# Kernel optimization log

Hardware: AMD Instinct MI355X
Metric: run time of the kernel (lower is better)

The kernel has to match this reference:

```python
import jax, jax.numpy as jnp
import numpy as np

B, N, C, ORDER, COORD, K = 2, 4096, 64, 4, 2, 8
EPS = 1e-8
LN_EPS = 1e-6


def _layer_norm(x, scale, bias):
    mu = jnp.mean(x, axis=-1, keepdims=True)
    var = jnp.mean(jnp.square(x - mu), axis=-1, keepdims=True)
    return (x - mu) * jax.lax.rsqrt(var + LN_EPS) * scale + bias


def _multipole(x, positions, W, order_scales, ln_s, ln_b):
    # stability clamping / NaN masking as in the original
    x = jnp.where(jnp.isnan(x), 0.0, jnp.clip(x, -1e6, 1e6))
    p = jnp.where(jnp.isnan(positions), 0.0, jnp.clip(positions, -1e6, 1e6))
    r = jnp.maximum(jnp.linalg.norm(p, axis=-1, keepdims=True), EPS)  # (B,N,1)
    theta = jnp.arctan2(p[..., 1], p[..., 0] + EPS)  # (B,N)
    per_order = []
    for o in range(ORDER + 1):
        r_o = r ** o
        radial = jnp.tanh(r_o / (1.0 + r_o))          # (B,N,1)
        angular = jnp.cos(o * theta)                    # (B,N)
        mc = x * radial * angular[..., None]            # (B,N,C)
        nm = mc / (jnp.linalg.norm(mc, axis=-1, keepdims=True) + EPS)
        scale = jnp.clip(order_scales[o], 0.01, 1.0)
        per_order.append(nm * scale / (o + 1.0))
    M = jnp.stack(per_order, axis=-1)  # (B,N,C,O+1) per-order weighted moments
    # per-order linear maps, summed over orders (evident intent of (C,C,O+1) weights)
    transformed = jnp.einsum('bnio,ijo->bnj', M, W)
    normalized = _layer_norm(transformed, ln_s, ln_b)
    return jnp.where(jnp.isnan(normalized), x, normalized)


def _local_messages(x, positions, W1, b1, W2, b2):
    # full pairwise distances, then kNN (exclude self)
    d = jnp.linalg.norm(positions[:, :, None, :] - positions[:, None, :, :], axis=-1)  # (B,N,N)
    _, idx = jax.lax.top_k(-d, K + 1)
    nbr = idx[:, :, 1:]  # (B,N,K)
    # gather neighbor features without materializing (B,N,N,C)
    nbr_feat = jax.vmap(lambda xb, ib: xb[ib])(x, nbr)           # (B,N,K,C)
    self_feat = jnp.broadcast_to(x[:, :, None, :], nbr_feat.shape)
    comb = jnp.concatenate([self_feat, nbr_feat], axis=-1)       # (B,N,K,2C)
    msg = jax.nn.gelu(comb @ W1 + b1) @ W2 + b2                  # (B,N,K,C)
    return jnp.mean(msg, axis=2)


def reference(x, positions, multipole_weights, order_scales, mp_ln_scale, mp_ln_bias,
              msg_W1, msg_b1, msg_W2, msg_b2, upd_W1, upd_b1, upd_W2, upd_b2,
              out_ln_scale, out_ln_bias):
    mp = _multipole(x, positions, multipole_weights, order_scales, mp_ln_scale, mp_ln_bias)
    lm = _local_messages(x, positions, msg_W1, msg_b1, msg_W2, msg_b2)
    u = jnp.concatenate([mp, lm], axis=-1)                       # (B,N,2C)
    upd = jax.nn.gelu(u @ upd_W1 + upd_b1) @ upd_W2 + upd_b2     # (B,N,C)
    return _layer_norm(x + upd, out_ln_scale, out_ln_bias)


def setup_inputs() -> dict:
    key = jax.random.key(0)
    ks = jax.random.split(key, 8)
    C2 = 2 * C
    xav = lambda k, shp: jax.random.normal(k, shp) * np.float32(np.sqrt(2.0 / (shp[0] + shp[-1])))
    return {
        'x': jax.random.normal(ks[0], (B, N, C), dtype=jnp.float32),
        'positions': jax.random.normal(ks[1], (B, N, COORD), dtype=jnp.float32),
        'multipole_weights': jax.random.normal(ks[2], (C, C, ORDER + 1)) * np.float32(0.1 / np.sqrt(ORDER + 1) * np.sqrt(1.0 / C)),
        'order_scales': jnp.ones(ORDER + 1) * 0.1,
        'mp_ln_scale': jnp.ones(C), 'mp_ln_bias': jnp.zeros(C),
        'msg_W1': xav(ks[3], (C2, C)), 'msg_b1': jnp.zeros(C),
        'msg_W2': xav(ks[4], (C, C)), 'msg_b2': jnp.zeros(C),
        'upd_W1': xav(ks[5], (C2, C2)), 'upd_b1': jnp.zeros(C2),
        'upd_W2': xav(ks[6], (C2, C)), 'upd_b2': jnp.zeros(C),
        'out_ln_scale': jnp.ones(C), 'out_ln_bias': jnp.zeros(C),
    }
```

## Files before the change

kernel.cpp:

```cpp
#include <hip/hip_runtime.h>
#include <math.h>

#define NNODES 4096
#define KNN 8
#define GX 64
#define NCELL (GX * GX)
#define BOX_LO (-4.5f)
#define CELL_INV (7.11111111f)

__device__ __forceinline__ int binf(float v) {
    int k = (int)floorf((v - BOX_LO) * CELL_INV);
    return min(GX - 1, max(0, k));
}

__device__ __forceinline__ float cleanf(float v) {
    if (v != v) return 0.0f;
    return fminf(fmaxf(v, -1.0e6f), 1.0e6f);
}

__device__ __forceinline__ float gelu_tanh(float v) {
    float v3 = v * v * v;
    float t = tanhf(0.7978845608028654f * (v + 0.044715f * v3));
    return 0.5f * v * (1.0f + t);
}

__device__ __forceinline__ float wave_sum64(float v) {
    #pragma unroll
    for (int off = 32; off > 0; off >>= 1)
        v += __shfl_xor(v, off, 64);
    return v;
}

__global__ __launch_bounds__(1024) void prep_kernel(
    const float* __restrict__ pos, float4* __restrict__ spk,
    int* __restrict__ boff,
    const float* __restrict__ mw,  const float* __restrict__ mW1,
    float* __restrict__ mWlt, float* __restrict__ mW1tA,
    float* __restrict__ mW1tB)
{
    __shared__ int cnt[NCELL];
    __shared__ int wsum[16], wexcl[16];

    if (blockIdx.x >= 2) {
        int tid = (blockIdx.x - 2) * 1024 + threadIdx.x;
        const int STEP = 6 * 1024;
        for (int g = tid; g < 5 * 64 * 64; g += STEP) {
            int o = g >> 12, rem = g & 4095, j = rem >> 6, i = rem & 63;
            mWlt[g] = mw[(i * 64 + j) * 5 + o];
        }
        for (int g = tid; g < 64 * 64; g += STEP) {
            int j = g >> 6, i = g & 63;
            mW1tA[g] = mW1[i * 64 + j];
            mW1tB[g] = mW1[(64 + i) * 64 + j];
        }
        return;
    }

    int b    = blockIdx.x;
    int t    = threadIdx.x;
    int wid  = t >> 6;
    int lane = t & 63;
    const float2* pb = (const float2*)(pos + (size_t)b * NNODES * 2);

    float qx[4], qy[4];
    int ck[4];
    #pragma unroll
    for (int s = 0; s < 4; ++s) cnt[t + s * 1024] = 0;
    __syncthreads();

    #pragma unroll
    for (int s = 0; s < 4; ++s) {
        float2 p = pb[t + s * 1024];
        qx[s] = cleanf(p.x); qy[s] = cleanf(p.y);
        ck[s] = binf(qy[s]) * GX + binf(qx[s]);
        atomicAdd(&cnt[ck[s]], 1);
    }
    __syncthreads();

    int c0 = cnt[4 * t], c1 = cnt[4 * t + 1], c2 = cnt[4 * t + 2], c3 = cnt[4 * t + 3];
    int s4 = c0 + c1 + c2 + c3;
    int sc = s4;
    #pragma unroll
    for (int off = 1; off < 64; off <<= 1) {
        int o = __shfl_up(sc, off, 64);
        if (lane >= off) sc += o;
    }
    if (lane == 63) wsum[wid] = sc;
    __syncthreads();
    if (t < 16) {
        int v = wsum[t];
        #pragma unroll
        for (int off = 1; off < 16; off <<= 1) {
            int o = __shfl_up(v, off, 64);
            if (t >= off) v += o;
        }
        wexcl[t] = v - wsum[t];
    }
    __syncthreads();
    int base = wexcl[wid] + (sc - s4);
    int* bofb = boff + b * (NCELL + 1);
    bofb[4 * t]     = base;
    bofb[4 * t + 1] = base + c0;
    bofb[4 * t + 2] = base + c0 + c1;
    bofb[4 * t + 3] = base + c0 + c1 + c2;
    if (t == 0) bofb[NCELL] = NNODES;
    cnt[4 * t]     = base;
    cnt[4 * t + 1] = base + c0;
    cnt[4 * t + 2] = base + c0 + c1;
    cnt[4 * t + 3] = base + c0 + c1 + c2;
    __syncthreads();

    #pragma unroll
    for (int s = 0; s < 4; ++s) {
        int p = atomicAdd(&cnt[ck[s]], 1);
        spk[(size_t)b * NNODES + p] =
            make_float4(qx[s], qy[s], __int_as_float(t + s * 1024), 0.0f);
    }
}

#define INSERT8(cur)                                                     \
    {                                                                    \
        unsigned long long c_ = (cur);                                   \
        _Pragma("unroll")                                                \
        for (int q_ = 0; q_ < 8; ++q_) {                                 \
            unsigned long long mn_ = (c_ < best[q_]) ? c_ : best[q_];    \
            c_ = (c_ < best[q_]) ? best[q_] : c_;                        \
            best[q_] = mn_;                                              \
        }                                                                \
    }

__global__ __launch_bounds__(512) void knn_kernel(
    const float* __restrict__ pos, const float4* __restrict__ spk,
    const int* __restrict__ boff, int* __restrict__ nbr)
{
    int wid  = threadIdx.x >> 6;
    int lane = threadIdx.x & 63;
    int row  = blockIdx.x * 8 + wid;
    int b    = row >> 12;
    int i    = row & 4095;

    const float4* sp = spk + (size_t)b * NNODES;
    const int*    bo = boff + b * (NCELL + 1);

    float2 pr = ((const float2*)(pos + (size_t)b * NNODES * 2))[i];
    float qx = cleanf(pr.x), qy = cleanf(pr.y);
    int qcx = binf(qx), qcy = binf(qy);

    unsigned long long best[8];
    #pragma unroll
    for (int q = 0; q < 8; ++q) best[q] = ~0ull;

    auto sweep = [&](int s0, int s1) {
        for (int p0 = s0; p0 < s1; p0 += 64) {
            int p = p0 + lane;
            bool valid = (p < s1);
            float4 cp = sp[min(p, s1 - 1)];
            int ci = __float_as_int(cp.z);
            float dx = qx - cp.x, dy = qy - cp.y;
            float d2 = __fadd_rn(__fmul_rn(dx, dx), __fmul_rn(dy, dy));
            unsigned long long cur =
                ((unsigned long long)__float_as_uint(d2) << 32) | (unsigned)ci;
            if (!valid || ci == i) cur = ~0ull;
            INSERT8(cur);
        }
    };

    int r = 1, cxL, cxH, cyL, cyH;
    for (;;) {
        cxL = max(qcx - r, 0); cxH = min(qcx + r, GX - 1);
        cyL = max(qcy - r, 0); cyH = min(qcy + r, GX - 1);
        int cnt = 0;
        for (int cy = cyL; cy <= cyH; ++cy)
            cnt += bo[cy * GX + cxH + 1] - bo[cy * GX + cxL];
        if (cnt >= 9 || (cxL == 0 && cxH == GX - 1 && cyL == 0 && cyH == GX - 1))
            break;
        r += (r < 4) ? 1 : (r >> 1);
    }
    for (int cy = cyL; cy <= cyH; ++cy)
        sweep(bo[cy * GX + cxL], bo[cy * GX + cxH + 1]);

    unsigned long long m8[8];
    #pragma unroll
    for (int rr = 0; rr < 8; ++rr) {
        unsigned long long k = best[0];
        #pragma unroll
        for (int off = 32; off > 0; off >>= 1) {
            unsigned long long o = __shfl_xor(k, off, 64);
            k = (o < k) ? o : k;
        }
        m8[rr] = k;
        if (best[0] == k) {
            #pragma unroll
            for (int q = 0; q < 7; ++q) best[q] = best[q + 1];
            best[7] = ~0ull;
        }
    }

    float U = __uint_as_float((unsigned)(m8[7] >> 32));
    float w = sqrtf(U) * 1.0001f + 1.0e-5f;
    int bxlo = binf(qx - w), bxhi = binf(qx + w);
    int bylo = binf(qy - w), byhi = binf(qy + w);

    #pragma unroll
    for (int q = 0; q < 8; ++q) best[q] = ~0ull;
    unsigned long long inj = m8[0];
    #pragma unroll
    for (int rr = 1; rr < 8; ++rr) inj = (lane == rr) ? m8[rr] : inj;
    if (lane < 8) best[0] = inj;

    for (int cy = bylo; cy <= byhi; ++cy) {
        int rl = bo[cy * GX + bxlo], rh = bo[cy * GX + bxhi + 1];
        if (cy >= cyL && cy <= cyH) {
            int e = bo[cy * GX + min(cxL, bxhi + 1)];
            sweep(rl, e);
            int s = bo[cy * GX + max(cxH + 1, bxlo)];
            sweep(s, rh);
        } else {
            sweep(rl, rh);
        }
    }

    unsigned out_j = 0;
    #pragma unroll
    for (int rr = 0; rr < 8; ++rr) {
        unsigned long long k = best[0];
        #pragma unroll
        for (int off = 32; off > 0; off >>= 1) {
            unsigned long long o = __shfl_xor(k, off, 64);
            k = (o < k) ? o : k;
        }
        if (lane == rr) out_j = (unsigned)k;
        if (best[0] == k) {
            #pragma unroll
            for (int q = 0; q < 7; ++q) best[q] = best[q + 1];
            best[7] = ~0ull;
        }
    }
    if (lane < 8) nbr[(size_t)row * KNN + lane] = (int)out_j;
}

__global__ __launch_bounds__(512) void multipole_gemm_kernel(
    const float* __restrict__ x, const float* __restrict__ pos,
    const float* __restrict__ mWlt, const float* __restrict__ mW1tA,
    const float* __restrict__ mW1tB, const float* __restrict__ osc,
    const float* __restrict__ lns, const float* __restrict__ lnb,
    float* __restrict__ mp, float* __restrict__ ab)
{
    __shared__ alignas(16) float Wl[5 * 64 * 68];
    __shared__ alignas(16) float WA[64 * 68];
    __shared__ alignas(16) float WB[64 * 68];
    __shared__ alignas(16) float xsh[32][68];
    __shared__ alignas(16) float xr[32][68];
    __shared__ float csh[32][5];
    int base = blockIdx.x * 32;

    for (int g = threadIdx.x; g < 5 * 64 * 16; g += 512) {
        int oj = g >> 4, i4 = (g & 15) * 4;
        *(float4*)&Wl[oj * 68 + i4] = *(const float4*)&mWlt[oj * 64 + i4];
    }
    for (int g = threadIdx.x; g < 64 * 16; g += 512) {
        int j = g >> 4, i4 = (g & 15) * 4;
        *(float4*)&WA[j * 68 + i4] = *(const float4*)&mW1tA[j * 64 + i4];
        *(float4*)&WB[j * 68 + i4] = *(const float4*)&mW1tB[j * 64 + i4];
    }
    for (int g = threadIdx.x; g < 32 * 64; g += 512) {
        float v = x[(size_t)base * 64 + g];
        xr[g >> 6][g & 63]  = v;
        xsh[g >> 6][g & 63] = cleanf(v);
    }
    __syncthreads();

    if (threadIdx.x < 32) {
        int t = threadIdx.x;
        float ss = 0.0f;
        for (int i = 0; i < 64; ++i) { float v = xsh[t][i]; ss += v * v; }
        float nx = sqrtf(ss);
        int node = base + t;
        float px = cleanf(pos[(size_t)node * 2]);
        float py = cleanf(pos[(size_t)node * 2 + 1]);
        float r = fmaxf(sqrtf(px * px + py * py), 1.0e-8f);
        float th = atan2f(py, px + 1.0e-8f);
        float r2 = r * r, r3 = r2 * r, r4 = r2 * r2;
        float ro[5] = {1.0f, r, r2, r3, r4};
        #pragma unroll
        for (int o = 0; o < 5; ++o) {
            float radial = tanhf(ro[o] / (1.0f + ro[o]));
            float ang = cosf((float)o * th);
            float s = radial * ang;
            float denom = fabsf(s) * nx + 1.0e-8f;
            float sc = fminf(fmaxf(osc[o], 0.01f), 1.0f);
            csh[t][o] = (s / denom) * sc / (float)(o + 1);
        }
    }
    __syncthreads();

    int w = threadIdx.x >> 6;
    int lane = threadIdx.x & 63;
    int nl0 = w * 4;

    float acc[4][5];
    float accA[4] = {0.f, 0.f, 0.f, 0.f};
    float accB[4] = {0.f, 0.f, 0.f, 0.f};
    #pragma unroll
    for (int r_ = 0; r_ < 4; ++r_)
        #pragma unroll
        for (int o = 0; o < 5; ++o) acc[r_][o] = 0.0f;

    #define MG_FMA(R, XI, XV, QC)                                          \
        { float xi_ = (XI), xv_ = (XV);                                    \
          acc[R][0] += xi_ * q0.QC; acc[R][1] += xi_ * q1.QC;              \
          acc[R][2] += xi_ * q2.QC; acc[R][3] += xi_ * q3.QC;              \
          acc[R][4] += xi_ * q4.QC;                                        \
          accA[R] += xv_ * qa.QC;  accB[R] += xv_ * qb.QC; }

    for (int i4 = 0; i4 < 64; i4 += 4) {
        float4 q0 = *(const float4*)&Wl[(0 * 64 + lane) * 68 + i4];
        float4 q1 = *(const float4*)&Wl[(1 * 64 + lane) * 68 + i4];
        float4 q2 = *(const float4*)&Wl[(2 * 64 + lane) * 68 + i4];
        float4 q3 = *(const float4*)&Wl[(3 * 64 + lane) * 68 + i4];
        float4 q4 = *(const float4*)&Wl[(4 * 64 + lane) * 68 + i4];
        float4 qa = *(const float4*)&WA[lane * 68 + i4];
        float4 qb = *(const float4*)&WB[lane * 68 + i4];
        #pragma unroll
        for (int r_ = 0; r_ < 4; ++r_) {
            float4 xc4 = *(const float4*)&xsh[nl0 + r_][i4];
            float4 xw4 = *(const float4*)&xr[nl0 + r_][i4];
            MG_FMA(r_, xc4.x, xw4.x, x)
            MG_FMA(r_, xc4.y, xw4.y, y)
            MG_FMA(r_, xc4.z, xw4.z, z)
            MG_FMA(r_, xc4.w, xw4.w, w)
        }
    }
    #undef MG_FMA

    float lnsv = lns[lane], lnbv = lnb[lane];
    #pragma unroll
    for (int r_ = 0; r_ < 4; ++r_) {
        int node = base + nl0 + r_;
        float tv = csh[nl0 + r_][0] * acc[r_][0] + csh[nl0 + r_][1] * acc[r_][1]
                 + csh[nl0 + r_][2] * acc[r_][2] + csh[nl0 + r_][3] * acc[r_][3]
                 + csh[nl0 + r_][4] * acc[r_][4];
        float mu = wave_sum64(tv) * (1.0f / 64.0f);
        float dv = tv - mu;
        float var = wave_sum64(dv * dv) * (1.0f / 64.0f);
        float o_ = dv * (1.0f / sqrtf(var + 1.0e-6f)) * lnsv + lnbv;
        if (o_ != o_) o_ = xsh[nl0 + r_][lane];
        mp[(size_t)node * 64 + lane] = o_;
        ab[(size_t)node * 128 + lane]      = accA[r_];
        ab[(size_t)node * 128 + 64 + lane] = accB[r_];
    }
}

__global__ __launch_bounds__(512) void msg_upd_kernel(
    const float* __restrict__ x, const float* __restrict__ ab,
    const int* __restrict__ nbr, const float* __restrict__ mp,
    const float* __restrict__ mb1, const float* __restrict__ mW2,
    const float* __restrict__ mb2,
    const float* __restrict__ uW1, const float* __restrict__ ub1,
    const float* __restrict__ uW2, const float* __restrict__ ub2,
    const float* __restrict__ lns, const float* __restrict__ lnb,
    float* __restrict__ out)
{
    __shared__ float W2l[64][64];
    __shared__ float W1u[128][128];
    __shared__ float W2u[128][64];
    __shared__ alignas(16) float ul[8][4][128];
    __shared__ alignas(16) float hl[8][4][128];
    int base = blockIdx.x * 32;

    for (int g = threadIdx.x; g < 64 * 64; g += 512)   ((float*)W2l)[g] = mW2[g];
    for (int g = threadIdx.x; g < 128 * 128; g += 512) ((float*)W1u)[g] = uW1[g];
    for (int g = threadIdx.x; g < 128 * 64; g += 512)  ((float*)W2u)[g] = uW2[g];
    __syncthreads();

    int w = threadIdx.x >> 6;
    int lane = threadIdx.x & 63;
    float b1m = mb1[lane], b2m = mb2[lane];
    float b1a = ub1[lane], b1b = ub1[lane + 64], b2u = ub2[lane];
    float lnsv = lns[lane], lnbv = lnb[lane];

    int node0 = base + w * 4;
    const float* abb = ab + (((size_t)(node0 >> 12)) << 12) * 128;
    const int* nb = nbr + (size_t)node0 * 8;

    float bvc[8];
    {
        int nb0[8];
        #pragma unroll
        for (int k = 0; k < 8; ++k) nb0[k] = nb[k];
        #pragma unroll
        for (int k = 0; k < 8; ++k)
            bvc[k] = abb[(size_t)nb0[k] * 128 + 64 + lane];
    }
    #pragma unroll
    for (int t = 0; t < 4; ++t) {
        int nbn[8];
        if (t < 3) {
            #pragma unroll
            for (int k = 0; k < 8; ++k) nbn[k] = nb[8 * (t + 1) + k];
        }
        float a = ab[(size_t)(node0 + t) * 128 + lane];
        float bvn[8];
        if (t < 3) {
            #pragma unroll
            for (int k = 0; k < 8; ++k)
                bvn[k] = abb[(size_t)nbn[k] * 128 + 64 + lane];
        }
        float hsum = 0.0f;
        #pragma unroll
        for (int k = 0; k < 8; ++k)
            hsum += gelu_tanh(a + bvc[k] + b1m);
        hl[w][t][lane] = hsum * 0.125f;
        #pragma unroll
        for (int k = 0; k < 8; ++k) bvc[k] = bvn[k];
    }

    float o_[4] = {0.f, 0.f, 0.f, 0.f};
    for (int h4 = 0; h4 < 64; h4 += 4) {
        float w0 = W2l[h4][lane],     w1 = W2l[h4 + 1][lane],
              w2 = W2l[h4 + 2][lane], w3 = W2l[h4 + 3][lane];
        #pragma unroll
        for (int r = 0; r < 4; ++r) {
            float4 hv = *(const float4*)&hl[w][r][h4];
            o_[r] += hv.x * w0 + hv.y * w1 + hv.z * w2 + hv.w * w3;
        }
    }

    #pragma unroll
    for (int r = 0; r < 4; ++r) {
        ul[w][r][lane]      = mp[(size_t)(node0 + r) * 64 + lane];
        ul[w][r][64 + lane] = o_[r] + b2m;
    }

    float h1a[4] = {0.f, 0.f, 0.f, 0.f}, h2a[4] = {0.f, 0.f, 0.f, 0.f};
    for (int i4 = 0; i4 < 128; i4 += 4) {
        float a0 = W1u[i4][lane],          a1 = W1u[i4 + 1][lane],
              a2 = W1u[i4 + 2][lane],      a3 = W1u[i4 + 3][lane];
        float c0 = W1u[i4][lane + 64],     c1 = W1u[i4 + 1][lane + 64],
              c2 = W1u[i4 + 2][lane + 64], c3 = W1u[i4 + 3][lane + 64];
        #pragma unroll
        for (int r = 0; r < 4; ++r) {
            float4 uv = *(const float4*)&ul[w][r][i4];
            h1a[r] += uv.x * a0 + uv.y * a1 + uv.z * a2 + uv.w * a3;
            h2a[r] += uv.x * c0 + uv.y * c1 + uv.z * c2 + uv.w * c3;
        }
    }
    #pragma unroll
    for (int r = 0; r < 4; ++r) {
        hl[w][r][lane]      = gelu_tanh(h1a[r] + b1a);
        hl[w][r][64 + lane] = gelu_tanh(h2a[r] + b1b);
    }

    float accq[4] = {0.f, 0.f, 0.f, 0.f};
    for (int h4 = 0; h4 < 128; h4 += 4) {
        float w0 = W2u[h4][lane],     w1 = W2u[h4 + 1][lane],
              w2 = W2u[h4 + 2][lane], w3 = W2u[h4 + 3][lane];
        #pragma unroll
        for (int r = 0; r < 4; ++r) {
            float4 hv = *(const float4*)&hl[w][r][h4];
            accq[r] += hv.x * w0 + hv.y * w1 + hv.z * w2 + hv.w * w3;
        }
    }

    #pragma unroll
    for (int r = 0; r < 4; ++r) {
        float pre = x[(size_t)(node0 + r) * 64 + lane] + accq[r] + b2u;
        float mu = wave_sum64(pre) * (1.0f / 64.0f);
        float dv = pre - mu;
        float var = wave_sum64(dv * dv) * (1.0f / 64.0f);
        out[(size_t)(node0 + r) * 64 + lane] =
            dv * (1.0f / sqrtf(var + 1.0e-6f)) * lnsv + lnbv;
    }
}

extern "C" void kernel_launch(void* const* d_in, const int* in_sizes, int n_in,
                              void* d_out, int out_size, void* d_ws, size_t ws_size,
                              hipStream_t stream)
{
    (void)in_sizes; (void)n_in; (void)out_size; (void)ws_size;
    const float* x     = (const float*)d_in[0];
    const float* pos   = (const float*)d_in[1];
    const float* mw    = (const float*)d_in[2];
    const float* osc   = (const float*)d_in[3];
    const float* mplns = (const float*)d_in[4];
    const float* mplnb = (const float*)d_in[5];
    const float* mW1   = (const float*)d_in[6];
    const float* mb1   = (const float*)d_in[7];
    const float* mW2   = (const float*)d_in[8];
    const float* mb2   = (const float*)d_in[9];
    const float* uW1   = (const float*)d_in[10];
    const float* ub1   = (const float*)d_in[11];
    const float* uW2   = (const float*)d_in[12];
    const float* ub2   = (const float*)d_in[13];
    const float* olns  = (const float*)d_in[14];
    const float* olnb  = (const float*)d_in[15];
    float* out = (float*)d_out;

    char* ws = (char*)d_ws;
    int*    nbr   = (int*)ws;
    float*  mp    = (float*)(ws + 262144);
    float*  ab    = (float*)(ws + 2359296);
    float4* spk   = (float4*)(ws + 6553600);
    int*    boff  = (int*)(ws + 6684672);
    float*  mWlt  = (float*)(ws + 6721536);
    float*  mW1tA = (float*)(ws + 6803456);
    float*  mW1tB = (float*)(ws + 6819840);

    prep_kernel<<<8, 1024, 0, stream>>>(pos, spk, boff,
        mw, mW1, mWlt, mW1tA, mW1tB);
    knn_kernel<<<1024, 512, 0, stream>>>(pos, spk, boff, nbr);
    multipole_gemm_kernel<<<256, 512, 0, stream>>>(
        x, pos, mWlt, mW1tA, mW1tB, osc, mplns, mplnb, mp, ab);
    msg_upd_kernel<<<256, 512, 0, stream>>>(
        x, ab, nbr, mp, mb1, mW2, mb2, uW1, ub1, uW2, ub2, olns, olnb, out);
}
```

Before: 84.13 us.

## Pack weights as float4 along reduction dim and early-exit kNN refine

The prep kernel now repacks all MLP and multipole weight matrices into float4-interleaved layouts, with four consecutive reduction rows per output column. The GEMM loops can then fetch one conflict-free 16-byte LDS load per lane instead of four scalar loads or padded strided float4s. The kNN kernel also skips the second sweep when the search radius stays inside the already-scanned cell window, writing the first-pass result directly. The cost is extra preprocessing work and workspace, and the correctness of the early exit depends on the coverage test.

Result: faster. 81.14 us (-3.6%).

```diff
diff --git a/kernel.cpp b/kernel.cpp
--- a/kernel.cpp
+++ b/kernel.cpp
@@ -35,8 +35,11 @@
     const float* __restrict__ pos, float4* __restrict__ spk,
     int* __restrict__ boff,
     const float* __restrict__ mw,  const float* __restrict__ mW1,
-    float* __restrict__ mWlt, float* __restrict__ mW1tA,
-    float* __restrict__ mW1tB)
+    const float* __restrict__ mW2, const float* __restrict__ uW1,
+    const float* __restrict__ uW2,
+    float4* __restrict__ mWltQ, float4* __restrict__ mW1tAQ,
+    float4* __restrict__ mW1tBQ, float4* __restrict__ uW1Q,
+    float4* __restrict__ uW2Q, float4* __restrict__ mW2Q)
 {
     __shared__ int cnt[NCELL];
     __shared__ int wsum[16], wexcl[16];
@@ -44,14 +47,46 @@
     if (blockIdx.x >= 2) {
         int tid = (blockIdx.x - 2) * 1024 + threadIdx.x;
         const int STEP = 6 * 1024;
-        for (int g = tid; g < 5 * 64 * 64; g += STEP) {
-            int o = g >> 12, rem = g & 4095, j = rem >> 6, i = rem & 63;
-            mWlt[g] = mw[(i * 64 + j) * 5 + o];
-        }
-        for (int g = tid; g < 64 * 64; g += STEP) {
-            int j = g >> 6, i = g & 63;
-            mW1tA[g] = mW1[i * 64 + j];
-            mW1tB[g] = mW1[(64 + i) * 64 + j];
+        for (int g = tid; g < 5 * 16 * 64; g += STEP) {
+            int o = g >> 10, rem = g & 1023, iq = rem >> 6, j = rem & 63;
+            float4 v;
+            v.x = mw[((4 * iq + 0) * 64 + j) * 5 + o];
+            v.y = mw[((4 * iq + 1) * 64 + j) * 5 + o];
+            v.z = mw[((4 * iq + 2) * 64 + j) * 5 + o];
+            v.w = mw[((4 * iq + 3) * 64 + j) * 5 + o];
+            mWltQ[g] = v;
+        }
+        for (int g = tid; g < 16 * 64; g += STEP) {
+            int iq = g >> 6, j = g & 63;
+            float4 a, b;
+            a.x = mW1[(4 * iq + 0) * 64 + j]; a.y = mW1[(4 * iq + 1) * 64 + j];
+            a.z = mW1[(4 * iq + 2) * 64 + j]; a.w = mW1[(4 * iq + 3) * 64 + j];
+            b.x = mW1[(64 + 4 * iq + 0) * 64 + j];
+            b.y = mW1[(64 + 4 * iq + 1) * 64 + j];
+            b.z = mW1[(64 + 4 * iq + 2) * 64 + j];
+            b.w = mW1[(64 + 4 * iq + 3) * 64 + j];
+            mW1tAQ[g] = a; mW1tBQ[g] = b;
+        }
+        for (int g = tid; g < 32 * 128; g += STEP) {
+            int iq = g >> 7, j = g & 127;
+            float4 v;
+            v.x = uW1[(4 * iq + 0) * 128 + j]; v.y = uW1[(4 * iq + 1) * 128 + j];
+            v.z = uW1[(4 * iq + 2) * 128 + j]; v.w = uW1[(4 * iq + 3) * 128 + j];
+            uW1Q[g] = v;
+        }
+        for (int g = tid; g < 32 * 64; g += STEP) {
+            int hq = g >> 6, j = g & 63;
+            float4 v;
+            v.x = uW2[(4 * hq + 0) * 64 + j]; v.y = uW2[(4 * hq + 1) * 64 + j];
+            v.z = uW2[(4 * hq + 2) * 64 + j]; v.w = uW2[(4 * hq + 3) * 64 + j];
+            uW2Q[g] = v;
+        }
+        for (int g = tid; g < 16 * 64; g += STEP) {
+            int hq = g >> 6, j = g & 63;
+            float4 v;
+            v.x = mW2[(4 * hq + 0) * 64 + j]; v.y = mW2[(4 * hq + 1) * 64 + j];
+            v.z = mW2[(4 * hq + 2) * 64 + j]; v.w = mW2[(4 * hq + 3) * 64 + j];
+            mW2Q[g] = v;
         }
         return;
     }
@@ -201,6 +236,14 @@
     int bxlo = binf(qx - w), bxhi = binf(qx + w);
     int bylo = binf(qy - w), byhi = binf(qy + w);
 
+    if (bxlo >= cxL && bxhi <= cxH && bylo >= cyL && byhi <= cyH) {
+        unsigned long long v = m8[0];
+        #pragma unroll
+        for (int rr = 1; rr < 8; ++rr) v = (lane == rr) ? m8[rr] : v;
+        if (lane < 8) nbr[(size_t)row * KNN + lane] = (int)(unsigned)v;
+        return;
+    }
+
     #pragma unroll
     for (int q = 0; q < 8; ++q) best[q] = ~0ull;
     unsigned long long inj = m8[0];
@@ -241,27 +284,23 @@
 
 __global__ __launch_bounds__(512) void multipole_gemm_kernel(
     const float* __restrict__ x, const float* __restrict__ pos,
-    const float* __restrict__ mWlt, const float* __restrict__ mW1tA,
-    const float* __restrict__ mW1tB, const float* __restrict__ osc,
+    const float4* __restrict__ mWltQ, const float4* __restrict__ mW1tAQ,
+    const float4* __restrict__ mW1tBQ, const float* __restrict__ osc,
     const float* __restrict__ lns, const float* __restrict__ lnb,
     float* __restrict__ mp, float* __restrict__ ab)
 {
-    __shared__ alignas(16) float Wl[5 * 64 * 68];
-    __shared__ alignas(16) float WA[64 * 68];
-    __shared__ alignas(16) float WB[64 * 68];
+    __shared__ alignas(16) float4 WlQ[5 * 16 * 64];
+    __shared__ alignas(16) float4 WAQ[16 * 64];
+    __shared__ alignas(16) float4 WBQ[16 * 64];
     __shared__ alignas(16) float xsh[32][68];
     __shared__ alignas(16) float xr[32][68];
     __shared__ float csh[32][5];
     int base = blockIdx.x * 32;
 
-    for (int g = threadIdx.x; g < 5 * 64 * 16; g += 512) {
-        int oj = g >> 4, i4 = (g & 15) * 4;
-        *(float4*)&Wl[oj * 68 + i4] = *(const float4*)&mWlt[oj * 64 + i4];
-    }
-    for (int g = threadIdx.x; g < 64 * 16; g += 512) {
-        int j = g >> 4, i4 = (g & 15) * 4;
-        *(float4*)&WA[j * 68 + i4] = *(const float4*)&mW1tA[j * 64 + i4];
-        *(float4*)&WB[j * 68 + i4] = *(const float4*)&mW1tB[j * 64 + i4];
+    for (int g = threadIdx.x; g < 5 * 16 * 64; g += 512) WlQ[g] = mWltQ[g];
+    for (int g = threadIdx.x; g < 16 * 64; g += 512) {
+        WAQ[g] = mW1tAQ[g];
+        WBQ[g] = mW1tBQ[g];
     }
     for (int g = threadIdx.x; g < 32 * 64; g += 512) {
         float v = x[(size_t)base * 64 + g];
@@ -314,13 +353,14 @@
           accA[R] += xv_ * qa.QC;  accB[R] += xv_ * qb.QC; }
 
     for (int i4 = 0; i4 < 64; i4 += 4) {
-        float4 q0 = *(const float4*)&Wl[(0 * 64 + lane) * 68 + i4];
-        float4 q1 = *(const float4*)&Wl[(1 * 64 + lane) * 68 + i4];
-        float4 q2 = *(const float4*)&Wl[(2 * 64 + lane) * 68 + i4];
-        float4 q3 = *(const float4*)&Wl[(3 * 64 + lane) * 68 + i4];
-        float4 q4 = *(const float4*)&Wl[(4 * 64 + lane) * 68 + i4];
-        float4 qa = *(const float4*)&WA[lane * 68 + i4];
-        float4 qb = *(const float4*)&WB[lane * 68 + i4];
+        int iq = i4 >> 2;
+        float4 q0 = WlQ[(0 * 16 + iq) * 64 + lane];
+        float4 q1 = WlQ[(1 * 16 + iq) * 64 + lane];
+        float4 q2 = WlQ[(2 * 16 + iq) * 64 + lane];
+        float4 q3 = WlQ[(3 * 16 + iq) * 64 + lane];
+        float4 q4 = WlQ[(4 * 16 + iq) * 64 + lane];
+        float4 qa = WAQ[iq * 64 + lane];
+        float4 qb = WBQ[iq * 64 + lane];
         #pragma unroll
         for (int r_ = 0; r_ < 4; ++r_) {
             float4 xc4 = *(const float4*)&xsh[nl0 + r_][i4];
@@ -354,23 +394,23 @@
 __global__ __launch_bounds__(512) void msg_upd_kernel(
     const float* __restrict__ x, const float* __restrict__ ab,
     const int* __restrict__ nbr, const float* __restrict__ mp,
-    const float* __restrict__ mb1, const float* __restrict__ mW2,
+    const float* __restrict__ mb1, const float4* __restrict__ mW2Q,
     const float* __restrict__ mb2,
-    const float* __restrict__ uW1, const float* __restrict__ ub1,
-    const float* __restrict__ uW2, const float* __restrict__ ub2,
+    const float4* __restrict__ uW1Q, const float* __restrict__ ub1,
+    const float4* __restrict__ uW2Q, const float* __restrict__ ub2,
     const float* __restrict__ lns, const float* __restrict__ lnb,
     float* __restrict__ out)
 {
-    __shared__ float W2l[64][64];
-    __shared__ float W1u[128][128];
-    __shared__ float W2u[128][64];
+    __shared__ alignas(16) float4 W1uQ[32 * 128];
+    __shared__ alignas(16) float4 W2uQ[32 * 64];
+    __shared__ alignas(16) float4 W2mQ[16 * 64];
     __shared__ alignas(16) float ul[8][4][128];
     __shared__ alignas(16) float hl[8][4][128];
     int base = blockIdx.x * 32;
 
-    for (int g = threadIdx.x; g < 64 * 64; g += 512)   ((float*)W2l)[g] = mW2[g];
-    for (int g = threadIdx.x; g < 128 * 128; g += 512) ((float*)W1u)[g] = uW1[g];
-    for (int g = threadIdx.x; g < 128 * 64; g += 512)  ((float*)W2u)[g] = uW2[g];
+    for (int g = threadIdx.x; g < 32 * 128; g += 512) W1uQ[g] = uW1Q[g];
+    for (int g = threadIdx.x; g < 32 * 64; g += 512)  W2uQ[g] = uW2Q[g];
+    for (int g = threadIdx.x; g < 16 * 64; g += 512)  W2mQ[g] = mW2Q[g];
     __syncthreads();
 
     int w = threadIdx.x >> 6;
@@ -417,12 +457,11 @@
 
     float o_[4] = {0.f, 0.f, 0.f, 0.f};
     for (int h4 = 0; h4 < 64; h4 += 4) {
-        float w0 = W2l[h4][lane],     w1 = W2l[h4 + 1][lane],
-              w2 = W2l[h4 + 2][lane], w3 = W2l[h4 + 3][lane];
+        float4 wq = W2mQ[(h4 >> 2) * 64 + lane];
         #pragma unroll
         for (int r = 0; r < 4; ++r) {
             float4 hv = *(const float4*)&hl[w][r][h4];
-            o_[r] += hv.x * w0 + hv.y * w1 + hv.z * w2 + hv.w * w3;
+            o_[r] += hv.x * wq.x + hv.y * wq.y + hv.z * wq.z + hv.w * wq.w;
         }
     }
 
@@ -434,15 +473,13 @@
 
     float h1a[4] = {0.f, 0.f, 0.f, 0.f}, h2a[4] = {0.f, 0.f, 0.f, 0.f};
     for (int i4 = 0; i4 < 128; i4 += 4) {
-        float a0 = W1u[i4][lane],          a1 = W1u[i4 + 1][lane],
-              a2 = W1u[i4 + 2][lane],      a3 = W1u[i4 + 3][lane];
-        float c0 = W1u[i4][lane + 64],     c1 = W1u[i4 + 1][lane + 64],
-              c2 = W1u[i4 + 2][lane + 64], c3 = W1u[i4 + 3][lane + 64];
+        float4 wA = W1uQ[(i4 >> 2) * 128 + lane];
+        float4 wC = W1uQ[(i4 >> 2) * 128 + lane + 64];
         #pragma unroll
         for (int r = 0; r < 4; ++r) {
             float4 uv = *(const float4*)&ul[w][r][i4];
-            h1a[r] += uv.x * a0 + uv.y * a1 + uv.z * a2 + uv.w * a3;
-            h2a[r] += uv.x * c0 + uv.y * c1 + uv.z * c2 + uv.w * c3;
+            h1a[r] += uv.x * wA.x + uv.y * wA.y + uv.z * wA.z + uv.w * wA.w;
+            h2a[r] += uv.x * wC.x + uv.y * wC.y + uv.z * wC.z + uv.w * wC.w;
         }
     }
     #pragma unroll
@@ -453,12 +490,11 @@
 
     float accq[4] = {0.f, 0.f, 0.f, 0.f};
     for (int h4 = 0; h4 < 128; h4 += 4) {
-        float w0 = W2u[h4][lane],     w1 = W2u[h4 + 1][lane],
-              w2 = W2u[h4 + 2][lane], w3 = W2u[h4 + 3][lane];
+        float4 wq = W2uQ[(h4 >> 2) * 64 + lane];
         #pragma unroll
         for (int r = 0; r < 4; ++r) {
             float4 hv = *(const float4*)&hl[w][r][h4];
-            accq[r] += hv.x * w0 + hv.y * w1 + hv.z * w2 + hv.w * w3;
+            accq[r] += hv.x * wq.x + hv.y * wq.y + hv.z * wq.z + hv.w * wq.w;
         }
     }
 
@@ -497,20 +533,23 @@
     float* out = (float*)d_out;
 
     char* ws = (char*)d_ws;
-    int*    nbr   = (int*)ws;
-    float*  mp    = (float*)(ws + 262144);
-    float*  ab    = (float*)(ws + 2359296);
-    float4* spk   = (float4*)(ws + 6553600);
-    int*    boff  = (int*)(ws + 6684672);
-    float*  mWlt  = (float*)(ws + 6721536);
-    float*  mW1tA = (float*)(ws + 6803456);
-    float*  mW1tB = (float*)(ws + 6819840);
+    int*    nbr    = (int*)ws;
+    float*  mp     = (float*)(ws + 262144);
+    float*  ab     = (float*)(ws + 2359296);
+    float4* spk    = (float4*)(ws + 6553600);
+    int*    boff   = (int*)(ws + 6684672);
+    float4* mWltQ  = (float4*)(ws + 6721536);
+    float4* mW1tAQ = (float4*)(ws + 6803456);
+    float4* mW1tBQ = (float4*)(ws + 6819840);
+    float4* uW1Q   = (float4*)(ws + 6836224);
+    float4* uW2Q   = (float4*)(ws + 6901760);
+    float4* mW2Q   = (float4*)(ws + 6934528);
 
     prep_kernel<<<8, 1024, 0, stream>>>(pos, spk, boff,
-        mw, mW1, mWlt, mW1tA, mW1tB);
+        mw, mW1, mW2, uW1, uW2, mWltQ, mW1tAQ, mW1tBQ, uW1Q, uW2Q, mW2Q);
     knn_kernel<<<1024, 512, 0, stream>>>(pos, spk, boff, nbr);
     multipole_gemm_kernel<<<256, 512, 0, stream>>>(
-        x, pos, mWlt, mW1tA, mW1tB, osc, mplns, mplnb, mp, ab);
+        x, pos, mWltQ, mW1tAQ, mW1tBQ, osc, mplns, mplnb, mp, ab);
     msg_upd_kernel<<<256, 512, 0, stream>>>(
-        x, ab, nbr, mp, mb1, mW2, mb2, uW1, ub1, uW2, ub2, olns, olnb, out);
-}
+        x, ab, nbr, mp, mb1, mW2Q, mb2, uW1Q, ub1, uW2Q, ub2, olns, olnb, out);
+}
```
